# Kernel tuning notes

Hardware: AMD Instinct MI355X
Metric: run time of the kernel (lower is better)

## Reference

```python
import jax, jax.numpy as jnp
import numpy as np

D = 1571  # NUM_CODE + 2
P = 128   # num_patient
T = 64    # visits per patient


def setup_inputs() -> dict:
    key = jax.random.key(0)
    k1, k2 = jax.random.split(key)
    N = P * T
    to_cut = jax.random.normal(k1, (P, T, D), dtype=jnp.float32)
    # per-visit kept lengths, in [1, D-1] so every visit keeps a nonempty prefix
    base = jax.random.randint(k2, (1, N), 1, D, dtype=jnp.int32)
    # visits grouped contiguously per patient (sorted ids), T visits each
    ids = jnp.repeat(jnp.arange(P, dtype=jnp.int32), T)
    return {"to_cut": to_cut, "base": base, "ids": ids}


def reference(to_cut, base, ids):
    """Dense equivalent of CutOutput: for each visit (p, t), take the descending
    argsort of scores and keep only the first L indices, where L is that visit's
    length from `base` (visit -> patient mapping given by sorted `ids`). Cut
    positions are zeroed (dense stand-in for the ragged strip in the original)."""
    Pp, Tt, Dd = to_cut.shape
    # descending-order code indices per visit  [P, T, D]
    order = jnp.argsort(-to_cut, axis=-1).astype(jnp.int32)
    N = ids.shape[0]
    # visits per patient and start offset of each patient's contiguous block
    counts = jax.ops.segment_sum(jnp.ones(N, jnp.int32), ids, num_segments=Pp)
    offsets = jnp.cumsum(counts) - counts
    j = jnp.arange(Tt, dtype=jnp.int32)
    idx = offsets[:, None] + j[None, :]              # [P, T] flat visit index
    valid = j[None, :] < counts[:, None]             # padded visits -> len 0
    lens = jnp.where(valid, base.reshape(-1)[jnp.clip(idx, 0, N - 1)], 0)  # [P, T]
    # keep top-L prefix per visit
    mask = jnp.arange(Dd, dtype=jnp.int32)[None, None, :] < lens[:, :, None]
    return order * mask.astype(jnp.int32)
```

## Files before the change

kernel.cpp:

```cpp
#include <hip/hip_runtime.h>
#include <stdint.h>


#define BLK 256
#define EPT 8

template<int RCT>
__global__ __launch_bounds__(BLK, 5) void cutout_radix_ct(
    const float* __restrict__ to_cut,
    const int*  __restrict__ base,
    int*        __restrict__ out,
    int D) {
  constexpr int MCT = RCT * 256;
  constexpr int WSH = RCT * 64;
  __shared__ uint32_t kbuf[2][MCT];
  __shared__ uint16_t ibuf[2][MCT];
  __shared__ uint32_t hist[4 * 256];
  __shared__ uint32_t sbuf[256];

  const int      t    = threadIdx.x;
  const int      lane = t & 63;
  const int      w    = t >> 6;
  const int      v    = blockIdx.x;
  const size_t   off  = (size_t)v * (size_t)D;
  const uint64_t lt   = (1ull << lane) - 1;

#pragma unroll
  for (int o = 0; o < RCT; ++o) {
    const int e = o * BLK + t;
    uint32_t key = 0xFFFFFFFFu;
    if (e < D) {
      uint32_t u = __float_as_uint(to_cut[off + e]);
      u = (u & 0x80000000u) ? ~u : (u | 0x80000000u);
      key = ~u;
    }
    kbuf[0][e] = key;
    ibuf[0][e] = (uint16_t)e;
  }

  int cur = 0;
#pragma unroll
  for (int pass = 0; pass < 4; ++pass) {
    const int  shift = 8 * pass;
    uint32_t*  kin   = kbuf[cur];
    uint16_t*  iin   = ibuf[cur];
    uint32_t*  kout  = kbuf[cur ^ 1];
    uint16_t*  iout  = ibuf[cur ^ 1];

#pragma unroll
    for (int q = 0; q < 4; ++q) hist[q * 256 + t] = 0;
    __syncthreads();

    uint32_t key[RCT], idx[RCT], dig[RCT], rnk[RCT];
#pragma unroll
    for (int o = 0; o < RCT; ++o) {
      const int pos = w * WSH + o * 64 + lane;
      key[o] = kin[pos];
      idx[o] = iin[pos];
      dig[o] = (key[o] >> shift) & 255u;
    }

#pragma unroll
    for (int o = 0; o < RCT; ++o) {
      uint64_t mm = ~0ull;
#pragma unroll
      for (int b = 0; b < 8; ++b) {
        const uint32_t bit = (dig[o] >> b) & 1u;
        const uint64_t bb  = __ballot(bit);
        mm &= bit ? bb : ~bb;
      }
      const uint32_t before = (uint32_t)__popcll(mm & lt);
      const uint32_t cnt    = (uint32_t)__popcll(mm);
      const uint32_t b0     = hist[w * 256 + dig[o]];
      if (before == 0) hist[w * 256 + dig[o]] = b0 + cnt;
      rnk[o] = b0 + before;
    }
    __syncthreads();

    sbuf[t] = hist[0 * 256 + t] + hist[1 * 256 + t] +
              hist[2 * 256 + t] + hist[3 * 256 + t];
    __syncthreads();
    if (t < 64) {
      const uint32_t c0 = sbuf[4 * t + 0], c1 = sbuf[4 * t + 1];
      const uint32_t c2 = sbuf[4 * t + 2], c3 = sbuf[4 * t + 3];
      const uint32_t s  = c0 + c1 + c2 + c3;
      uint32_t vs = s;
#pragma unroll
      for (int d = 1; d < 64; d <<= 1) {
        const uint32_t u2 = __shfl_up(vs, d, 64);
        if (lane >= d) vs += u2;
      }
      const uint32_t ex = vs - s;
      sbuf[4 * t + 0] = ex;
      sbuf[4 * t + 1] = ex + c0;
      sbuf[4 * t + 2] = ex + c0 + c1;
      sbuf[4 * t + 3] = ex + c0 + c1 + c2;
    }
    __syncthreads();
    {
      const uint32_t c0 = hist[0 * 256 + t], c1 = hist[1 * 256 + t];
      const uint32_t c2 = hist[2 * 256 + t];
      uint32_t run = sbuf[t];
      hist[0 * 256 + t] = run; run += c0;
      hist[1 * 256 + t] = run; run += c1;
      hist[2 * 256 + t] = run; run += c2;
      hist[3 * 256 + t] = run;
    }
    __syncthreads();

#pragma unroll
    for (int o = 0; o < RCT; ++o) {
      const uint32_t dest = hist[w * 256 + dig[o]] + rnk[o];
      kout[dest] = key[o];
      iout[dest] = (uint16_t)idx[o];
    }
    cur ^= 1;
  }
  __syncthreads();

  const int L = base[v];
#pragma unroll
  for (int o = 0; o < RCT; ++o) {
    const int r = o * BLK + t;
    if (r < D) out[off + r] = (r < L) ? (int)ibuf[0][r] : 0;
  }
}

extern "C" void kernel_launch(void* const* d_in, const int* in_sizes, int n_in,
                              void* d_out, int out_size, void* d_ws, size_t ws_size,
                              hipStream_t stream) {
  const float* to_cut = (const float*)d_in[0];
  const int*   base   = (const int*)d_in[1];
  const int N = in_sizes[1];
  const int D = in_sizes[0] / N;

  int* outp = (int*)d_out;
  const int R = ((D + 255) & ~255) >> 8;
  switch (R) {
    case 1: cutout_radix_ct<1><<<dim3(N), dim3(BLK), 0, stream>>>(to_cut, base, outp, D); break;
    case 2: cutout_radix_ct<2><<<dim3(N), dim3(BLK), 0, stream>>>(to_cut, base, outp, D); break;
    case 3: cutout_radix_ct<3><<<dim3(N), dim3(BLK), 0, stream>>>(to_cut, base, outp, D); break;
    case 4: cutout_radix_ct<4><<<dim3(N), dim3(BLK), 0, stream>>>(to_cut, base, outp, D); break;
    case 5: cutout_radix_ct<5><<<dim3(N), dim3(BLK), 0, stream>>>(to_cut, base, outp, D); break;
    case 6: cutout_radix_ct<6><<<dim3(N), dim3(BLK), 0, stream>>>(to_cut, base, outp, D); break;
    case 7: cutout_radix_ct<7><<<dim3(N), dim3(BLK), 0, stream>>>(to_cut, base, outp, D); break;
    default: cutout_radix_ct<8><<<dim3(N), dim3(BLK), 0, stream>>>(to_cut, base, outp, D); break;
  }
}
```

Before: 206.1 us.

## Sort on top 16 key bits with two radix passes plus insertion-sort tie fixup

Replaces the four-pass 8-bit LSD radix sort with two passes over the upper 16 bits of the float key, packing the element index into the low 16 bits of each word. Runs of equal upper-16-bit keys are then fixed up by a per-thread insertion sort that compares the full key, reading the stored low halves from shared memory. This halves the number of ballot/scan/scatter passes and drops the separate index buffer, which cuts shared memory and lets occupancy rise to 6 blocks per unit. In exchange it adds serial fixup work whose cost depends on how many keys collide in their top bits, and for random normals with about 1571 elements collisions are rare.

```diff
diff --git a/kernel.cpp b/kernel.cpp
--- a/kernel.cpp
+++ b/kernel.cpp
@@ -3,18 +3,78 @@
 
 
 #define BLK 256
-#define EPT 8
 
 template<int RCT>
-__global__ __launch_bounds__(BLK, 5) void cutout_radix_ct(
+__device__ __forceinline__ void rank_scan_scatter(
+    uint32_t* __restrict__ hist, uint32_t* __restrict__ sbuf,
+    uint32_t* __restrict__ kout,
+    const uint32_t (&pk)[RCT], const uint32_t (&dig)[RCT],
+    const int t, const int lane, const int w, const uint64_t lt) {
+  uint32_t rnk[RCT];
+#pragma unroll
+  for (int o = 0; o < RCT; ++o) {
+    uint64_t mm = ~0ull;
+#pragma unroll
+    for (int b = 0; b < 8; ++b) {
+      const uint32_t bit = (dig[o] >> b) & 1u;
+      const uint64_t bb  = __ballot(bit);
+      mm &= bit ? bb : ~bb;
+    }
+    const uint32_t before = (uint32_t)__popcll(mm & lt);
+    const uint32_t cnt    = (uint32_t)__popcll(mm);
+    const uint32_t b0     = hist[w * 256 + dig[o]];
+    if (before == 0) hist[w * 256 + dig[o]] = b0 + cnt;
+    rnk[o] = b0 + before;
+  }
+  __syncthreads();
+
+  sbuf[t] = hist[0 * 256 + t] + hist[1 * 256 + t] +
+            hist[2 * 256 + t] + hist[3 * 256 + t];
+  __syncthreads();
+  if (t < 64) {
+    const uint32_t c0 = sbuf[4 * t + 0], c1 = sbuf[4 * t + 1];
+    const uint32_t c2 = sbuf[4 * t + 2], c3 = sbuf[4 * t + 3];
+    const uint32_t s  = c0 + c1 + c2 + c3;
+    uint32_t vs = s;
+#pragma unroll
+    for (int d = 1; d < 64; d <<= 1) {
+      const uint32_t u2 = __shfl_up(vs, d, 64);
+      if (lane >= d) vs += u2;
+    }
+    const uint32_t ex = vs - s;
+    sbuf[4 * t + 0] = ex;
+    sbuf[4 * t + 1] = ex + c0;
+    sbuf[4 * t + 2] = ex + c0 + c1;
+    sbuf[4 * t + 3] = ex + c0 + c1 + c2;
+  }
+  __syncthreads();
+  {
+    const uint32_t c0 = hist[0 * 256 + t], c1 = hist[1 * 256 + t];
+    const uint32_t c2 = hist[2 * 256 + t];
+    uint32_t run = sbuf[t];
+    hist[0 * 256 + t] = run; run += c0;
+    hist[1 * 256 + t] = run; run += c1;
+    hist[2 * 256 + t] = run; run += c2;
+    hist[3 * 256 + t] = run;
+  }
+  __syncthreads();
+
+#pragma unroll
+  for (int o = 0; o < RCT; ++o)
+    kout[hist[w * 256 + dig[o]] + rnk[o]] = pk[o];
+}
+
+template<int RCT>
+__global__ __launch_bounds__(BLK, 6) void cutout_radix16(
     const float* __restrict__ to_cut,
     const int*  __restrict__ base,
     int*        __restrict__ out,
     int D) {
   constexpr int MCT = RCT * 256;
   constexpr int WSH = RCT * 64;
-  __shared__ uint32_t kbuf[2][MCT];
-  __shared__ uint16_t ibuf[2][MCT];
+  __shared__ uint32_t kA[MCT];
+  __shared__ uint32_t kB[MCT];
+  __shared__ uint16_t lowb[MCT];
   __shared__ uint32_t hist[4 * 256];
   __shared__ uint32_t sbuf[256];
 
@@ -26,95 +86,61 @@
   const uint64_t lt   = (1ull << lane) - 1;
 
 #pragma unroll
+  for (int q = 0; q < 4; ++q) hist[q * 256 + t] = 0;
+  __syncthreads();
+
+  uint32_t pk[RCT], dig[RCT];
+#pragma unroll
   for (int o = 0; o < RCT; ++o) {
-    const int e = o * BLK + t;
-    uint32_t key = 0xFFFFFFFFu;
-    if (e < D) {
-      uint32_t u = __float_as_uint(to_cut[off + e]);
+    const int p = w * WSH + o * 64 + lane;
+    uint32_t packed = 0xFFFF0000u | (uint32_t)p;
+    if (p < D) {
+      uint32_t u = __float_as_uint(to_cut[off + p]);
       u = (u & 0x80000000u) ? ~u : (u | 0x80000000u);
-      key = ~u;
+      const uint32_t key = ~u;
+      packed = (key & 0xFFFF0000u) | (uint32_t)p;
+      lowb[p] = (uint16_t)(key & 0xFFFFu);
     }
-    kbuf[0][e] = key;
-    ibuf[0][e] = (uint16_t)e;
+    pk[o]  = packed;
+    dig[o] = (packed >> 16) & 255u;
   }
-
-  int cur = 0;
-#pragma unroll
-  for (int pass = 0; pass < 4; ++pass) {
-    const int  shift = 8 * pass;
-    uint32_t*  kin   = kbuf[cur];
-    uint16_t*  iin   = ibuf[cur];
-    uint32_t*  kout  = kbuf[cur ^ 1];
-    uint16_t*  iout  = ibuf[cur ^ 1];
+  rank_scan_scatter<RCT>(hist, sbuf, kB, pk, dig, t, lane, w, lt);
+  __syncthreads();
 
 #pragma unroll
-    for (int q = 0; q < 4; ++q) hist[q * 256 + t] = 0;
-    __syncthreads();
-
-    uint32_t key[RCT], idx[RCT], dig[RCT], rnk[RCT];
+  for (int q = 0; q < 4; ++q) hist[q * 256 + t] = 0;
+  __syncthreads();
 #pragma unroll
-    for (int o = 0; o < RCT; ++o) {
-      const int pos = w * WSH + o * 64 + lane;
-      key[o] = kin[pos];
-      idx[o] = iin[pos];
-      dig[o] = (key[o] >> shift) & 255u;
-    }
+  for (int o = 0; o < RCT; ++o) {
+    const int p = w * WSH + o * 64 + lane;
+    pk[o]  = kB[p];
+    dig[o] = pk[o] >> 24;
+  }
+  rank_scan_scatter<RCT>(hist, sbuf, kA, pk, dig, t, lane, w, lt);
+  __syncthreads();
 
 #pragma unroll
-    for (int o = 0; o < RCT; ++o) {
-      uint64_t mm = ~0ull;
-#pragma unroll
-      for (int b = 0; b < 8; ++b) {
-        const uint32_t bit = (dig[o] >> b) & 1u;
-        const uint64_t bb  = __ballot(bit);
-        mm &= bit ? bb : ~bb;
+  for (int o = 0; o < RCT; ++o) {
+    const int r = o * BLK + t;
+    const uint32_t k16 = kA[r] >> 16;
+    if (k16 == 0xFFFFu) continue;
+    if (r + 1 >= MCT || (kA[r + 1] >> 16) != k16) continue;
+    if (r > 0 && (kA[r - 1] >> 16) == k16) continue;
+    int e = r + 2;
+    while (e < MCT && (kA[e] >> 16) == k16) ++e;
+    for (int i = r + 1; i < e; ++i) {
+      const uint32_t wi = kA[i];
+      const uint32_t ci = ((uint32_t)lowb[wi & 0xFFFFu] << 16) | (wi & 0xFFFFu);
+      int j = i - 1;
+      while (j >= r) {
+        const uint32_t wj = kA[j];
+        const uint32_t cj = ((uint32_t)lowb[wj & 0xFFFFu] << 16) | (wj & 0xFFFFu);
+        if (cj <= ci) break;
+        kA[j + 1] = wj;
+        --j;
       }
-      const uint32_t before = (uint32_t)__popcll(mm & lt);
-      const uint32_t cnt    = (uint32_t)__popcll(mm);
-      const uint32_t b0     = hist[w * 256 + dig[o]];
-      if (before == 0) hist[w * 256 + dig[o]] = b0 + cnt;
-      rnk[o] = b0 + before;
+      kA[j + 1] = wi;
     }
-    __syncthreads();
-
-    sbuf[t] = hist[0 * 256 + t] + hist[1 * 256 + t] +
-              hist[2 * 256 + t] + hist[3 * 256 + t];
-    __syncthreads();
-    if (t < 64) {
-      const uint32_t c0 = sbuf[4 * t + 0], c1 = sbuf[4 * t + 1];
-      const uint32_t c2 = sbuf[4 * t + 2], c3 = sbuf[4 * t + 3];
-      const uint32_t s  = c0 + c1 + c2 + c3;
-      uint32_t vs = s;
-#pragma unroll
-      for (int d = 1; d < 64; d <<= 1) {
-        const uint32_t u2 = __shfl_up(vs, d, 64);
-        if (lane >= d) vs += u2;
-      }
-      const uint32_t ex = vs - s;
-      sbuf[4 * t + 0] = ex;
-      sbuf[4 * t + 1] = ex + c0;
-      sbuf[4 * t + 2] = ex + c0 + c1;
-      sbuf[4 * t + 3] = ex + c0 + c1 + c2;
-    }
-    __syncthreads();
-    {
-      const uint32_t c0 = hist[0 * 256 + t], c1 = hist[1 * 256 + t];
-      const uint32_t c2 = hist[2 * 256 + t];
-      uint32_t run = sbuf[t];
-      hist[0 * 256 + t] = run; run += c0;
-      hist[1 * 256 + t] = run; run += c1;
-      hist[2 * 256 + t] = run; run += c2;
-      hist[3 * 256 + t] = run;
-    }
-    __syncthreads();
-
-#pragma unroll
-    for (int o = 0; o < RCT; ++o) {
-      const uint32_t dest = hist[w * 256 + dig[o]] + rnk[o];
-      kout[dest] = key[o];
-      iout[dest] = (uint16_t)idx[o];
-    }
-    cur ^= 1;
   }
   __syncthreads();
 
@@ -122,7 +148,7 @@
 #pragma unroll
   for (int o = 0; o < RCT; ++o) {
     const int r = o * BLK + t;
-    if (r < D) out[off + r] = (r < L) ? (int)ibuf[0][r] : 0;
+    if (r < D) out[off + r] = (r < L) ? (int)(kA[r] & 0xFFFFu) : 0;
   }
 }
 
@@ -137,13 +163,13 @@
   int* outp = (int*)d_out;
   const int R = ((D + 255) & ~255) >> 8;
   switch (R) {
-    case 1: cutout_radix_ct<1><<<dim3(N), dim3(BLK), 0, stream>>>(to_cut, base, outp, D); break;
-    case 2: cutout_radix_ct<2><<<dim3(N), dim3(BLK), 0, stream>>>(to_cut, base, outp, D); break;
-    case 3: cutout_radix_ct<3><<<dim3(N), dim3(BLK), 0, stream>>>(to_cut, base, outp, D); break;
-    case 4: cutout_radix_ct<4><<<dim3(N), dim3(BLK), 0, stream>>>(to_cut, base, outp, D); break;
-    case 5: cutout_radix_ct<5><<<dim3(N), dim3(BLK), 0, stream>>>(to_cut, base, outp, D); break;
-    case 6: cutout_radix_ct<6><<<dim3(N), dim3(BLK), 0, stream>>>(to_cut, base, outp, D); break;
-    case 7: cutout_radix_ct<7><<<dim3(N), dim3(BLK), 0, stream>>>(to_cut, base, outp, D); break;
-    default: cutout_radix_ct<8><<<dim3(N), dim3(BLK), 0, stream>>>(to_cut, base, outp, D); break;
+    case 1: cutout_radix16<1><<<dim3(N), dim3(BLK), 0, stream>>>(to_cut, base, outp, D); break;
+    case 2: cutout_radix16<2><<<dim3(N), dim3(BLK), 0, stream>>>(to_cut, base, outp, D); break;
+    case 3: cutout_radix16<3><<<dim3(N), dim3(BLK), 0, stream>>>(to_cut, base, outp, D); break;
+    case 4: cutout_radix16<4><<<dim3(N), dim3(BLK), 0, stream>>>(to_cut, base, outp, D); break;
+    case 5: cutout_radix16<5><<<dim3(N), dim3(BLK), 0, stream>>>(to_cut, base, outp, D); break;
+    case 6: cutout_radix16<6><<<dim3(N), dim3(BLK), 0, stream>>>(to_cut, base, outp, D); break;
+    case 7: cutout_radix16<7><<<dim3(N), dim3(BLK), 0, stream>>>(to_cut, base, outp, D); break;
+    default: cutout_radix16<8><<<dim3(N), dim3(BLK), 0, stream>>>(to_cut, base, outp, D); break;
   }
 }
```

Measured after the change: 219.2 us. 1.06x slower.
